# Performance work log

Hardware: AMD Instinct MI355X
Metric: run time of the kernel (lower is better)

Reference implementation:

```python
import jax, jax.numpy as jnp
import numpy as np

NUM_BUCKETS = 32
MAX_DISTANCE = 128
N_HEADS = 16
D_KV = 64


def relative_position_bucket(rel, num_buckets=NUM_BUCKETS, max_distance=MAX_DISTANCE):
    # bidirectional (encoder) bucketing, matches the torch reference
    nb = num_buckets // 2
    ret = (rel > 0).astype(jnp.int32) * nb
    rp = jnp.abs(rel)
    max_exact = nb // 2
    is_small = rp < max_exact
    # guard log(0); masked out by is_small anyway
    large = max_exact + (
        jnp.log(jnp.maximum(rp, 1).astype(jnp.float32) / max_exact)
        / np.log(max_distance / max_exact)
        * (nb - max_exact)
    ).astype(jnp.int32)
    large = jnp.minimum(large, nb - 1)
    return ret + jnp.where(is_small, rp, large)


def compute_bias(rel_bias_table, q_len, k_len):
    q_pos = jnp.arange(q_len)[:, None]
    k_pos = jnp.arange(k_len)[None, :]
    buckets = relative_position_bucket(k_pos - q_pos)  # [S, K]
    bias = rel_bias_table[buckets]                      # [S, K, H]
    return jnp.transpose(bias, (2, 0, 1))[None]         # [1, H, S, K]


def setup_inputs() -> dict:
    key = jax.random.key(0)
    ks = jax.random.split(key, 6)
    d_model, inner = 1024, N_HEADS * D_KV
    scale = 1.0 / np.sqrt(d_model)
    return {
        "hidden_states": jax.random.normal(ks[0], (4, 2048, d_model), jnp.float32),
        "Wq": jax.random.normal(ks[1], (d_model, inner), jnp.float32) * scale,
        "Wk": jax.random.normal(ks[2], (d_model, inner), jnp.float32) * scale,
        "Wv": jax.random.normal(ks[3], (d_model, inner), jnp.float32) * scale,
        "Wo": jax.random.normal(ks[4], (inner, d_model), jnp.float32) * scale,
        "rel_bias_table": jax.random.normal(ks[5], (NUM_BUCKETS, N_HEADS), jnp.float32),
    }


def reference(hidden_states, Wq, Wk, Wv, Wo, rel_bias_table):
    B, S, _ = hidden_states.shape
    K_len = S  # self-attention (key_value_states is None)
    q = (hidden_states @ Wq).reshape(B, S, N_HEADS, D_KV)
    k = (hidden_states @ Wk).reshape(B, K_len, N_HEADS, D_KV)
    v = (hidden_states @ Wv).reshape(B, K_len, N_HEADS, D_KV)
    # NOTE: T5 attention has no 1/sqrt(d_kv) scaling
    scores = jnp.einsum("bshd,bkhd->bhsk", q, k)
    pos_bias = compute_bias(rel_bias_table, S, K_len)
    attn = jax.nn.softmax(scores + pos_bias, axis=-1)
    out = jnp.einsum("bhsk,bkhd->bshd", attn, v).reshape(B, S, N_HEADS * D_KV)
    out = out @ Wo
    return (out, pos_bias)
```

## Files before the change

### kernel.cpp

```cpp
#include <hip/hip_runtime.h>
#include <cstdint>
#include <cstddef>

typedef unsigned short u16;
typedef unsigned int u32;
typedef __attribute__((ext_vector_type(8))) short bf16x8;
typedef __attribute__((ext_vector_type(4))) float f32x4;

#define MFMA(a, b, c) __builtin_amdgcn_mfma_f32_16x16x32_bf16((a), (b), (c), 0, 0, 0)

typedef const __attribute__((address_space(1))) void gv1_t;
typedef __attribute__((address_space(3))) void lv3_t;
#define GLOAD_LDS16(g, l) __builtin_amdgcn_global_load_lds((gv1_t*)(g), (lv3_t*)(l), 16, 0, 0)

#define BATCH 4
#define SEQ 2048
#define DMODEL 1024
#define NHEAD 16
#define MROWS (BATCH * SEQ)
#define QKVN (3 * DMODEL)

#define LOG2E 1.44269504088896340736f

__device__ __forceinline__ u16 f2bf(float f) {
  u32 x = __builtin_bit_cast(u32, f);
  x += 0x7fffu + ((x >> 16) & 1u);
  return (u16)(x >> 16);
}

__device__ __forceinline__ u32 pkbf(float a, float b) {
  return (u32)f2bf(a) | ((u32)f2bf(b) << 16);
}

extern "C" __device__ float __ocml_exp2_f32(float);
__device__ __forceinline__ float exp2fast(float x) {
#if __has_builtin(__builtin_amdgcn_exp2f)
  return __builtin_amdgcn_exp2f(x);
#else
  return __ocml_exp2_f32(x);
#endif
}

__device__ __forceinline__ float xqsum(float v) {
  v += __shfl_xor(v, 16);
  return v + __shfl_xor(v, 32);
}

__global__ __launch_bounds__(256) void convert_h(const float* __restrict__ H,
                                                 u16* __restrict__ Hb) {
  size_t i = (size_t)blockIdx.x * 1024 + threadIdx.x * 4;
  float4 v = *(const float4*)&H[i];
  uint2 o;
  o.x = pkbf(v.x, v.y);
  o.y = pkbf(v.z, v.w);
  *(uint2*)&Hb[i] = o;
}

__global__ void transpose_w(const float* __restrict__ Wq, const float* __restrict__ Wk,
                            const float* __restrict__ Wv, const float* __restrict__ Wo,
                            u16* __restrict__ Wt) {
  __shared__ u16 Ts[32][33];
  const float* W = (blockIdx.z == 0) ? Wq : (blockIdx.z == 1) ? Wk
                   : (blockIdx.z == 2) ? Wv : Wo;
  const float s = (blockIdx.z == 0) ? LOG2E : 1.0f;
  int x = threadIdx.x, y0 = threadIdx.y;
  int r0 = blockIdx.y * 32, c0 = blockIdx.x * 32;
  for (int yy = y0; yy < 32; yy += 8)
    Ts[yy][x] = f2bf(W[(size_t)(r0 + yy) * 1024 + c0 + x] * s);
  __syncthreads();
  for (int yy = y0; yy < 32; yy += 8)
    Wt[(size_t)(blockIdx.z * 1024 + c0 + yy) * 1024 + r0 + x] = Ts[x][yy];
}

__device__ __forceinline__ int rel_bucket(int rel) {
  int ret = (rel > 0) ? 16 : 0;
  int rp = (rel < 0) ? -rel : rel;
  if (rp < 8) return ret + rp;
  int i = 0;
  i += (rp >= 12); i += (rp >= 16); i += (rp >= 23); i += (rp >= 32);
  i += (rp >= 46); i += (rp >= 64); i += (rp >= 91);
  return ret + 8 + i;
}

__global__ __launch_bounds__(256) void build_bias_rel(const float* __restrict__ tbl,
                                                      float* __restrict__ brel,
                                                      float* __restrict__ brel2) {
  int h = blockIdx.x;
  for (int rix = threadIdx.x; rix < 4095; rix += 256) {
    float v = tbl[rel_bucket(rix - 2047) * NHEAD + h];
    brel[h * 4096 + rix] = v;
    brel2[h * 4096 + rix] = v * LOG2E;
  }
}

__global__ __launch_bounds__(256) void gemm_bf16k(const u16* __restrict__ A,
                                                  const u16* __restrict__ Bt,
                                                  u16* __restrict__ Cb, float* __restrict__ Cf,
                                                  int M, int N, int K) {
  __shared__ u16 As[128 * 32];
  __shared__ u16 Bs[128 * 32];
  const int t = threadIdx.x;
  const int w = t >> 6, lane = t & 63, quad = lane >> 4, l15 = lane & 15;
  const int wr = w >> 1, wc = w & 1;
  const int row0 = blockIdx.y * 128, col0 = blockIdx.x * 128;

  f32x4 acc[4][4];
  #pragma unroll
  for (int i = 0; i < 4; ++i)
    #pragma unroll
    for (int j = 0; j < 4; ++j) acc[i][j] = (f32x4){0.f, 0.f, 0.f, 0.f};

  const int srow = lane >> 2, scol = (lane & 3) * 8;

  for (int k0 = 0; k0 < K; k0 += 32) {
    #pragma unroll
    for (int p = 0; p < 2; ++p) {
      const int rb = w * 32 + p * 16;
      GLOAD_LDS16(&A[(size_t)(row0 + rb + srow) * K + k0 + scol], &As[rb * 32]);
      GLOAD_LDS16(&Bt[(size_t)(col0 + rb + srow) * K + k0 + scol], &Bs[rb * 32]);
    }
    __syncthreads();
    bf16x8 af[4], bfr[4];
    #pragma unroll
    for (int i = 0; i < 4; ++i)
      af[i] = *(const bf16x8*)&As[(wr * 64 + i * 16 + l15) * 32 + quad * 8];
    #pragma unroll
    for (int j = 0; j < 4; ++j)
      bfr[j] = *(const bf16x8*)&Bs[(wc * 64 + j * 16 + l15) * 32 + quad * 8];
    #pragma unroll
    for (int i = 0; i < 4; ++i)
      #pragma unroll
      for (int j = 0; j < 4; ++j)
        acc[i][j] = MFMA(af[i], bfr[j], acc[i][j]);
    __syncthreads();
  }
  #pragma unroll
  for (int i = 0; i < 4; ++i) {
    #pragma unroll
    for (int j = 0; j < 4; ++j) {
      int col = col0 + wc * 64 + j * 16 + l15;
      #pragma unroll
      for (int r = 0; r < 4; ++r) {
        int row = row0 + wr * 64 + i * 16 + quad * 4 + r;
        if (Cb) Cb[(size_t)row * N + col] = f2bf(acc[i][j][r]);
        else    Cf[(size_t)row * N + col] = acc[i][j][r];
      }
    }
  }
}

__global__ __launch_bounds__(256) void transpose_v(const u16* __restrict__ QKV,
                                                   u16* __restrict__ Vt) {
  __shared__ u16 Ts[64 * 72];
  int st = blockIdx.x, bh = blockIdx.y;
  int b = bh >> 4, h = bh & 15;
  int t = threadIdx.x;
  #pragma unroll
  for (int p = 0; p < 2; ++p) {
    int c = t * 2 + p, r = c >> 3, cc = (c & 7) * 8;
    *(uint4*)&Ts[r * 72 + cc] =
        *(const uint4*)&QKV[(size_t)(b * SEQ + st * 64 + r) * QKVN + 2 * DMODEL + h * 64 + cc];
  }
  __syncthreads();
  #pragma unroll
  for (int p = 0; p < 2; ++p) {
    int c = t * 2 + p, d = c >> 3, s8 = (c & 7) * 8;
    union { u16 u[8]; uint4 v; } tmp;
    #pragma unroll
    for (int jj = 0; jj < 8; ++jj) tmp.u[jj] = Ts[(s8 + jj) * 72 + d];
    *(uint4*)&Vt[((size_t)(bh * 64 + d)) * SEQ + st * 64 + s8] = tmp.v;
  }
}

__global__ __launch_bounds__(256) void attn_fused(const u16* __restrict__ QKV,
                                                  const u16* __restrict__ Vt,
                                                  const float* __restrict__ brel,
                                                  const float* __restrict__ brel2,
                                                  u16* __restrict__ Aout,
                                                  float* __restrict__ pb) {
  __shared__ u16 Ks[64 * 72];
  __shared__ u16 Vs[64 * 72];
  __shared__ u16 Ps[4][16 * 72];
  const int qt = blockIdx.x, bh = blockIdx.y;
  const int b = bh >> 4, h = bh & 15;
  const int t = threadIdx.x;
  const int w = t >> 6, lane = t & 63, quad = lane >> 4, l15 = lane & 15;
  const int q0 = qt * 64 + w * 16;
  const bool wrbias = (bh < 16);

  const float cpos = brel2[h * 4096 + 4040];
  const float cneg = brel2[h * 4096 + 54];
  const float cpu  = brel[h * 4096 + 4040];
  const float cnu  = brel[h * 4096 + 54];

  const u16* qptr = QKV + (size_t)(b * SEQ + q0 + l15) * QKVN + h * 64 + quad * 8;
  bf16x8 aq0 = *(const bf16x8*)qptr;
  bf16x8 aq1 = *(const bf16x8*)(qptr + 32);

  float lsum = 0.f;
  f32x4 oacc[4];
  #pragma unroll
  for (int j = 0; j < 4; ++j) oacc[j] = (f32x4){0.f, 0.f, 0.f, 0.f};

  const int c0 = t * 2, c1 = c0 + 1;
  const int r0s = c0 >> 3, cc0 = (c0 & 7) * 8;
  const int r1s = c1 >> 3, cc1 = (c1 & 7) * 8;
  const size_t krow = (size_t)(b * SEQ) * QKVN + DMODEL + h * 64;
  const size_t vtrow = (size_t)bh * 64;
  const float* brow = brel2 + h * 4096 + 2047;
  const int dbias = quad * 4 - q0 - l15;
  u16* Pw = Ps[w];

  uint4 ka0 = *(const uint4*)&QKV[krow + (size_t)r0s * QKVN + cc0];
  uint4 ka1 = *(const uint4*)&QKV[krow + (size_t)r1s * QKVN + cc1];
  uint4 va0 = *(const uint4*)&Vt[(vtrow + r0s) * SEQ + cc0];
  uint4 va1 = *(const uint4*)&Vt[(vtrow + r1s) * SEQ + cc1];

  for (int kb = 0; kb < SEQ; kb += 64) {
    *(uint4*)&Ks[r0s * 72 + cc0] = ka0;
    *(uint4*)&Ks[r1s * 72 + cc1] = ka1;
    *(uint4*)&Vs[r0s * 72 + cc0] = va0;
    *(uint4*)&Vs[r1s * 72 + cc1] = va1;
    __syncthreads();

    if (kb + 64 < SEQ) {
      ka0 = *(const uint4*)&QKV[krow + (size_t)(kb + 64 + r0s) * QKVN + cc0];
      ka1 = *(const uint4*)&QKV[krow + (size_t)(kb + 64 + r1s) * QKVN + cc1];
      va0 = *(const uint4*)&Vt[(vtrow + r0s) * SEQ + kb + 64 + cc0];
      va1 = *(const uint4*)&Vt[(vtrow + r1s) * SEQ + kb + 64 + cc1];
    }

    f32x4 sc[4];
    #pragma unroll
    for (int j = 0; j < 4; ++j) {
      bf16x8 bk0 = *(const bf16x8*)&Ks[(j * 16 + l15) * 72 + quad * 8];
      bf16x8 bk1 = *(const bf16x8*)&Ks[(j * 16 + l15) * 72 + 32 + quad * 8];
      f32x4 z = (f32x4){0.f, 0.f, 0.f, 0.f};
      z = MFMA(bk0, aq0, z);
      z = MFMA(bk1, aq1, z);
      sc[j] = z;
    }

    const bool fastp = (kb >= q0 + 106);
    const bool fastn = (kb + 154 <= q0);

    if (wrbias) {
      float* po = pb + ((size_t)(h * SEQ + q0 + l15)) * SEQ + kb + quad * 16;
      if (fastp || fastn) {
        const float c = fastp ? cpu : cnu;
        const float4 vv = {c, c, c, c};
        #pragma unroll
        for (int i = 0; i < 4; ++i) *(float4*)&po[i * 4] = vv;
      } else {
        const float* bb = brel + h * 4096 + 2047 - (q0 + l15) + kb + quad * 16;
        #pragma unroll
        for (int i = 0; i < 4; ++i) {
          float4 vv;
          vv.x = bb[i * 4]; vv.y = bb[i * 4 + 1];
          vv.z = bb[i * 4 + 2]; vv.w = bb[i * 4 + 3];
          *(float4*)&po[i * 4] = vv;
        }
      }
    }

    if (fastp | fastn) {
      const float cb = fastp ? cpos : cneg;
      #pragma unroll
      for (int j = 0; j < 4; ++j)
        #pragma unroll
        for (int r = 0; r < 4; ++r) sc[j][r] += cb;
    } else {
      #pragma unroll
      for (int j = 0; j < 4; ++j)
        #pragma unroll
        for (int r = 0; r < 4; ++r)
          sc[j][r] += brow[kb + j * 16 + r + dbias];
    }

    #pragma unroll
    for (int j = 0; j < 4; ++j) {
      float p0 = exp2fast(sc[j][0]);
      float p1 = exp2fast(sc[j][1]);
      float p2 = exp2fast(sc[j][2]);
      float p3 = exp2fast(sc[j][3]);
      lsum += (p0 + p1) + (p2 + p3);
      uint2 pk;
      pk.x = pkbf(p0, p1);
      pk.y = pkbf(p2, p3);
      *(uint2*)&Pw[l15 * 72 + j * 16 + quad * 4] = pk;
    }

    asm volatile("s_waitcnt lgkmcnt(0)" ::: "memory");
    bf16x8 bp0 = *(const bf16x8*)&Pw[l15 * 72 + quad * 8];
    bf16x8 bp1 = *(const bf16x8*)&Pw[l15 * 72 + 32 + quad * 8];
    #pragma unroll
    for (int j2 = 0; j2 < 4; ++j2) {
      bf16x8 av0 = *(const bf16x8*)&Vs[(j2 * 16 + l15) * 72 + quad * 8];
      bf16x8 av1 = *(const bf16x8*)&Vs[(j2 * 16 + l15) * 72 + 32 + quad * 8];
      oacc[j2] = MFMA(av0, bp0, oacc[j2]);
      oacc[j2] = MFMA(av1, bp1, oacc[j2]);
    }
    __syncthreads();
  }

  const float inv = 1.0f / xqsum(lsum);
  const size_t rowb = (size_t)(b * SEQ + q0 + l15) * DMODEL + h * 64;
  #pragma unroll
  for (int j2 = 0; j2 < 4; ++j2) {
    uint2 o;
    o.x = pkbf(oacc[j2][0] * inv, oacc[j2][1] * inv);
    o.y = pkbf(oacc[j2][2] * inv, oacc[j2][3] * inv);
    *(uint2*)&Aout[rowb + j2 * 16 + quad * 4] = o;
  }
}

extern "C" void kernel_launch(void* const* d_in, const int* in_sizes, int n_in,
                              void* d_out, int out_size, void* d_ws, size_t ws_size,
                              hipStream_t stream) {
  (void)in_sizes; (void)n_in; (void)out_size; (void)ws_size;
  const float* H   = (const float*)d_in[0];
  const float* Wq  = (const float*)d_in[1];
  const float* Wk  = (const float*)d_in[2];
  const float* Wv  = (const float*)d_in[3];
  const float* Wo  = (const float*)d_in[4];
  const float* tbl = (const float*)d_in[5];

  float* out = (float*)d_out;
  float* pos_bias = out + (size_t)MROWS * DMODEL;

  char* ws = (char*)d_ws;
  u16* Hb     = (u16*)(ws);
  u16* Wt     = (u16*)(ws + 16777216);
  u16* QKV    = (u16*)(ws + 25165824);
  u16* Vt     = (u16*)(ws + 75497472);
  float* brel  = (float*)(ws + 92274688);
  float* brel2 = (float*)(ws + 92536832);

  convert_h<<<8192, 256, 0, stream>>>(H, Hb);
  transpose_w<<<dim3(32, 32, 4), dim3(32, 8), 0, stream>>>(Wq, Wk, Wv, Wo, Wt);
  build_bias_rel<<<16, 256, 0, stream>>>(tbl, brel, brel2);

  gemm_bf16k<<<dim3(QKVN / 128, MROWS / 128), 256, 0, stream>>>(
      Hb, Wt, QKV, nullptr, MROWS, QKVN, DMODEL);
  transpose_v<<<dim3(32, 64), 256, 0, stream>>>(QKV, Vt);
  attn_fused<<<dim3(32, 64), 256, 0, stream>>>(QKV, Vt, brel, brel2,
                                               Hb , pos_bias);
  gemm_bf16k<<<dim3(DMODEL / 128, MROWS / 128), 256, 0, stream>>>(
      Hb, Wt + (size_t)QKVN * DMODEL, nullptr, out, MROWS, DMODEL, DMODEL);
}
```

Baseline: 604.8 us.

## Switch attention to 32x32x16 MFMA with 128-query tiles per block

Each wave now handles 32 query rows instead of 16, using 32x32x16 bf16 MFMAs for both QK^T and PV, and each block covers 128 queries, so the grid halves. Every K/V tile loaded into LDS is reused by twice as many queries, cutting global K/V traffic and the number of barriers per query. The bias fast-path thresholds and pos_bias write mapping are recomputed for the new tiling. This raises register use (f32x16 accumulators) and halves the block count, which may lower occupancy and parallelism.

New measurement: 603.4 us. About the same (-0.2%).

```diff
diff --git a/kernel.cpp b/kernel.cpp
--- a/kernel.cpp
+++ b/kernel.cpp
@@ -6,8 +6,10 @@
 typedef unsigned int u32;
 typedef __attribute__((ext_vector_type(8))) short bf16x8;
 typedef __attribute__((ext_vector_type(4))) float f32x4;
-
-#define MFMA(a, b, c) __builtin_amdgcn_mfma_f32_16x16x32_bf16((a), (b), (c), 0, 0, 0)
+typedef __attribute__((ext_vector_type(16))) float f32x16;
+
+#define MFMA(a, b, c)   __builtin_amdgcn_mfma_f32_16x16x32_bf16((a), (b), (c), 0, 0, 0)
+#define MFMA32(a, b, c) __builtin_amdgcn_mfma_f32_32x32x16_bf16((a), (b), (c), 0, 0, 0)
 
 typedef const __attribute__((address_space(1))) void gv1_t;
 typedef __attribute__((address_space(3))) void lv3_t;
@@ -39,11 +41,6 @@
 #else
   return __ocml_exp2_f32(x);
 #endif
-}
-
-__device__ __forceinline__ float xqsum(float v) {
-  v += __shfl_xor(v, 16);
-  return v + __shfl_xor(v, 32);
 }
 
 __global__ __launch_bounds__(256) void convert_h(const float* __restrict__ H,
@@ -180,12 +177,14 @@
                                                   float* __restrict__ pb) {
   __shared__ u16 Ks[64 * 72];
   __shared__ u16 Vs[64 * 72];
-  __shared__ u16 Ps[4][16 * 72];
+  __shared__ u16 Ps[4][32 * 72];
   const int qt = blockIdx.x, bh = blockIdx.y;
   const int b = bh >> 4, h = bh & 15;
   const int t = threadIdx.x;
-  const int w = t >> 6, lane = t & 63, quad = lane >> 4, l15 = lane & 15;
-  const int q0 = qt * 64 + w * 16;
+  const int w = t >> 6, lane = t & 63, l31 = lane & 31, h5 = lane >> 5;
+  const int qb = qt * 128;
+  const int qw0 = qb + w * 32;
+  const int qr = qw0 + l31;
   const bool wrbias = (bh < 16);
 
   const float cpos = brel2[h * 4096 + 4040];
@@ -193,14 +192,17 @@
   const float cpu  = brel[h * 4096 + 4040];
   const float cnu  = brel[h * 4096 + 54];
 
-  const u16* qptr = QKV + (size_t)(b * SEQ + q0 + l15) * QKVN + h * 64 + quad * 8;
-  bf16x8 aq0 = *(const bf16x8*)qptr;
-  bf16x8 aq1 = *(const bf16x8*)(qptr + 32);
+  const u16* qptr = QKV + (size_t)(b * SEQ + qr) * QKVN + h * 64 + h5 * 8;
+  bf16x8 qf[4];
+  #pragma unroll
+  for (int ks = 0; ks < 4; ++ks) qf[ks] = *(const bf16x8*)(qptr + ks * 16);
 
   float lsum = 0.f;
-  f32x4 oacc[4];
-  #pragma unroll
-  for (int j = 0; j < 4; ++j) oacc[j] = (f32x4){0.f, 0.f, 0.f, 0.f};
+  f32x16 oacc[2];
+  #pragma unroll
+  for (int m = 0; m < 2; ++m)
+    #pragma unroll
+    for (int i = 0; i < 16; ++i) oacc[m][i] = 0.f;
 
   const int c0 = t * 2, c1 = c0 + 1;
   const int r0s = c0 >> 3, cc0 = (c0 & 7) * 8;
@@ -208,7 +210,6 @@
   const size_t krow = (size_t)(b * SEQ) * QKVN + DMODEL + h * 64;
   const size_t vtrow = (size_t)bh * 64;
   const float* brow = brel2 + h * 4096 + 2047;
-  const int dbias = quad * 4 - q0 - l15;
   u16* Pw = Ps[w];
 
   uint4 ka0 = *(const uint4*)&QKV[krow + (size_t)r0s * QKVN + cc0];
@@ -230,31 +231,32 @@
       va1 = *(const uint4*)&Vt[(vtrow + r1s) * SEQ + kb + 64 + cc1];
     }
 
-    f32x4 sc[4];
-    #pragma unroll
-    for (int j = 0; j < 4; ++j) {
-      bf16x8 bk0 = *(const bf16x8*)&Ks[(j * 16 + l15) * 72 + quad * 8];
-      bf16x8 bk1 = *(const bf16x8*)&Ks[(j * 16 + l15) * 72 + 32 + quad * 8];
-      f32x4 z = (f32x4){0.f, 0.f, 0.f, 0.f};
-      z = MFMA(bk0, aq0, z);
-      z = MFMA(bk1, aq1, z);
-      sc[j] = z;
-    }
-
-    const bool fastp = (kb >= q0 + 106);
-    const bool fastn = (kb + 154 <= q0);
+    f32x16 sc[2];
+    #pragma unroll
+    for (int m = 0; m < 2; ++m) {
+      #pragma unroll
+      for (int i = 0; i < 16; ++i) sc[m][i] = 0.f;
+      #pragma unroll
+      for (int ks = 0; ks < 4; ++ks) {
+        bf16x8 kf = *(const bf16x8*)&Ks[(m * 32 + l31) * 72 + ks * 16 + h5 * 8];
+        sc[m] = MFMA32(kf, qf[ks], sc[m]);
+      }
+    }
 
     if (wrbias) {
-      float* po = pb + ((size_t)(h * SEQ + q0 + l15)) * SEQ + kb + quad * 16;
-      if (fastp || fastn) {
-        const float c = fastp ? cpu : cnu;
+      const int pr = qb + (t >> 1);
+      const int pc = kb + (t & 1) * 32;
+      float* po = pb + ((size_t)(h * SEQ + pr)) * SEQ + pc;
+      const int lo = pc - pr;
+      if (lo >= 91 || lo + 31 <= -91) {
+        const float c = (lo >= 91) ? cpu : cnu;
         const float4 vv = {c, c, c, c};
         #pragma unroll
-        for (int i = 0; i < 4; ++i) *(float4*)&po[i * 4] = vv;
+        for (int i = 0; i < 8; ++i) *(float4*)&po[i * 4] = vv;
       } else {
-        const float* bb = brel + h * 4096 + 2047 - (q0 + l15) + kb + quad * 16;
-        #pragma unroll
-        for (int i = 0; i < 4; ++i) {
+        const float* bb = brel + h * 4096 + 2047 - pr + pc;
+        #pragma unroll
+        for (int i = 0; i < 8; ++i) {
           float4 vv;
           vv.x = bb[i * 4]; vv.y = bb[i * 4 + 1];
           vv.z = bb[i * 4 + 2]; vv.w = bb[i * 4 + 3];
@@ -263,55 +265,61 @@
       }
     }
 
-    if (fastp | fastn) {
-      const float cb = fastp ? cpos : cneg;
-      #pragma unroll
-      for (int j = 0; j < 4; ++j)
-        #pragma unroll
-        for (int r = 0; r < 4; ++r) sc[j][r] += cb;
-    } else {
-      #pragma unroll
-      for (int j = 0; j < 4; ++j)
-        #pragma unroll
-        for (int r = 0; r < 4; ++r)
-          sc[j][r] += brow[kb + j * 16 + r + dbias];
-    }
-
-    #pragma unroll
-    for (int j = 0; j < 4; ++j) {
-      float p0 = exp2fast(sc[j][0]);
-      float p1 = exp2fast(sc[j][1]);
-      float p2 = exp2fast(sc[j][2]);
-      float p3 = exp2fast(sc[j][3]);
-      lsum += (p0 + p1) + (p2 + p3);
-      uint2 pk;
-      pk.x = pkbf(p0, p1);
-      pk.y = pkbf(p2, p3);
-      *(uint2*)&Pw[l15 * 72 + j * 16 + quad * 4] = pk;
+    #pragma unroll
+    for (int m = 0; m < 2; ++m) {
+      const int kb32 = kb + 32 * m;
+      if (kb32 >= qw0 + 122) {
+        #pragma unroll
+        for (int i = 0; i < 16; ++i) sc[m][i] += cpos;
+      } else if (kb32 <= qw0 - 122) {
+        #pragma unroll
+        for (int i = 0; i < 16; ++i) sc[m][i] += cneg;
+      } else {
+        const float* bb = brow + kb32 + 4 * h5 - qr;
+        #pragma unroll
+        for (int i = 0; i < 16; ++i) sc[m][i] += bb[(i & 3) + 8 * (i >> 2)];
+      }
+      #pragma unroll
+      for (int tt = 0; tt < 4; ++tt) {
+        float p0 = exp2fast(sc[m][4 * tt + 0]);
+        float p1 = exp2fast(sc[m][4 * tt + 1]);
+        float p2 = exp2fast(sc[m][4 * tt + 2]);
+        float p3 = exp2fast(sc[m][4 * tt + 3]);
+        lsum += (p0 + p1) + (p2 + p3);
+        uint2 pk;
+        pk.x = pkbf(p0, p1);
+        pk.y = pkbf(p2, p3);
+        *(uint2*)&Pw[l31 * 72 + 32 * m + 8 * tt + 4 * h5] = pk;
+      }
     }
 
     asm volatile("s_waitcnt lgkmcnt(0)" ::: "memory");
-    bf16x8 bp0 = *(const bf16x8*)&Pw[l15 * 72 + quad * 8];
-    bf16x8 bp1 = *(const bf16x8*)&Pw[l15 * 72 + 32 + quad * 8];
-    #pragma unroll
-    for (int j2 = 0; j2 < 4; ++j2) {
-      bf16x8 av0 = *(const bf16x8*)&Vs[(j2 * 16 + l15) * 72 + quad * 8];
-      bf16x8 av1 = *(const bf16x8*)&Vs[(j2 * 16 + l15) * 72 + 32 + quad * 8];
-      oacc[j2] = MFMA(av0, bp0, oacc[j2]);
-      oacc[j2] = MFMA(av1, bp1, oacc[j2]);
-    }
+    bf16x8 bp[4];
+    #pragma unroll
+    for (int ks = 0; ks < 4; ++ks)
+      bp[ks] = *(const bf16x8*)&Pw[l31 * 72 + ks * 16 + h5 * 8];
+    #pragma unroll
+    for (int m2 = 0; m2 < 2; ++m2)
+      #pragma unroll
+      for (int ks = 0; ks < 4; ++ks) {
+        bf16x8 vf = *(const bf16x8*)&Vs[(m2 * 32 + l31) * 72 + ks * 16 + h5 * 8];
+        oacc[m2] = MFMA32(vf, bp[ks], oacc[m2]);
+      }
     __syncthreads();
   }
 
-  const float inv = 1.0f / xqsum(lsum);
-  const size_t rowb = (size_t)(b * SEQ + q0 + l15) * DMODEL + h * 64;
-  #pragma unroll
-  for (int j2 = 0; j2 < 4; ++j2) {
-    uint2 o;
-    o.x = pkbf(oacc[j2][0] * inv, oacc[j2][1] * inv);
-    o.y = pkbf(oacc[j2][2] * inv, oacc[j2][3] * inv);
-    *(uint2*)&Aout[rowb + j2 * 16 + quad * 4] = o;
-  }
+  lsum += __shfl_xor(lsum, 32);
+  const float inv = 1.0f / lsum;
+  const size_t rowb = (size_t)(b * SEQ + qr) * DMODEL + h * 64;
+  #pragma unroll
+  for (int m2 = 0; m2 < 2; ++m2)
+    #pragma unroll
+    for (int tt = 0; tt < 4; ++tt) {
+      uint2 o;
+      o.x = pkbf(oacc[m2][4 * tt + 0] * inv, oacc[m2][4 * tt + 1] * inv);
+      o.y = pkbf(oacc[m2][4 * tt + 2] * inv, oacc[m2][4 * tt + 3] * inv);
+      *(uint2*)&Aout[rowb + 32 * m2 + 8 * tt + 4 * h5] = o;
+    }
 }
 
 extern "C" void kernel_launch(void* const* d_in, const int* in_sizes, int n_in,
@@ -343,7 +351,7 @@
   gemm_bf16k<<<dim3(QKVN / 128, MROWS / 128), 256, 0, stream>>>(
       Hb, Wt, QKV, nullptr, MROWS, QKVN, DMODEL);
   transpose_v<<<dim3(32, 64), 256, 0, stream>>>(QKV, Vt);
-  attn_fused<<<dim3(32, 64), 256, 0, stream>>>(QKV, Vt, brel, brel2,
+  attn_fused<<<dim3(16, 64), 256, 0, stream>>>(QKV, Vt, brel, brel2,
                                                Hb , pos_bias);
   gemm_bf16k<<<dim3(DMODEL / 128, MROWS / 128), 256, 0, stream>>>(
       Hb, Wt + (size_t)QKVN * DMODEL, nullptr, out, MROWS, DMODEL, DMODEL);
```
